# Kernel tuning notes

Measured on AMD Instinct MI355X. Metric: run time of the kernel, lower is better.

The kernel has to match this reference:

```python
import jax, jax.numpy as jnp
import numpy as np

N_SRC, N_TGT, E = 50000, 50000, 1600000
SRC_IN, TGT_IN, H, L = 64, 64, 128, 3
N = N_SRC + N_TGT


def setup_inputs() -> dict:
    key = jax.random.key(0)
    ks = jax.random.split(key, 12)
    s = 1.0 / np.sqrt(H)
    return {
        "src_x": jax.random.normal(ks[0], (N_SRC, SRC_IN), jnp.float32),
        "tgt_x": jax.random.normal(ks[1], (N_TGT, TGT_IN), jnp.float32),
        "edge_index": jax.random.randint(ks[2], (2, E), 0, N, jnp.int32),
        "Wsrc": jax.random.normal(ks[3], (H, SRC_IN), jnp.float32) / np.sqrt(SRC_IN),
        "bsrc": jnp.zeros((H,), jnp.float32),
        "Wtgt": jax.random.normal(ks[4], (H, TGT_IN), jnp.float32) / np.sqrt(TGT_IN),
        "btgt": jnp.zeros((H,), jnp.float32),
        "Wl": jax.random.normal(ks[5], (L, H, H), jnp.float32) * s,  # neighbor-aggregate weight
        "bl": jnp.zeros((L, H), jnp.float32),
        "Wr": jax.random.normal(ks[6], (L, H, H), jnp.float32) * s,  # root (self) weight, no bias
    }


def reference(src_x, tgt_x, edge_index, Wsrc, bsrc, Wtgt, btgt, Wl, bl, Wr):
    src_idx, dst_idx = edge_index[0], edge_index[1]
    # input projections + concat over node dim
    x = jnp.concatenate([src_x @ Wsrc.T + bsrc, tgt_x @ Wtgt.T + btgt], axis=0)  # [N,H]
    # in-degree for mean aggregation (computed once; edge structure is fixed)
    deg = jax.ops.segment_sum(jnp.ones((E,), x.dtype), dst_idx, num_segments=N)
    inv_deg = (1.0 / jnp.maximum(deg, 1.0))[:, None]  # [N,1]
    h = x
    for i in range(L):
        msg = h[src_idx]  # gather: [E,H]
        agg = jax.ops.segment_sum(msg, dst_idx, num_segments=N) * inv_deg  # mean aggr
        # PyG SAGEConv: lin_l(mean_neighbors) + lin_r(self); lin_l has bias
        h = agg @ Wl[i].T + bl[i] + h @ Wr[i].T
        if i + 1 < L:
            h = jax.nn.relu(h)  # dropout p=0.0 (eval) -> identity
    return h
```

## Files before the change

kernel.cpp:

```cpp
#include <hip/hip_runtime.h>
#include <hip/hip_fp8.h>

#define NSRC 50000
#define NTGT 50000
#define NTOT 100000
#define NE   1600000
#define IND  64
#define HD   128
#define CAP  64
#define CHUNK2 2048
#define NCH2 784
#define SBIN 128
#define NBIN 782
#define NBINP 784
#define PROJB 391
#define PACKB 48

typedef short s16x8 __attribute__((ext_vector_type(8)));
typedef float f32x4 __attribute__((ext_vector_type(4)));

__device__ __forceinline__ ushort f2bf(float f) {
  union { float f; uint u; } v; v.f = f;
  const uint r = v.u + 0x7fffu + ((v.u >> 16) & 1u);
  return (ushort)(r >> 16);
}
__device__ __forceinline__ float bfl(uint v) {
  union { uint u; float f; } c; c.u = v << 16; return c.f;
}
__device__ __forceinline__ float bfh(uint v) {
  union { uint u; float f; } c; c.u = v & 0xffff0000u; return c.f;
}
__device__ __forceinline__ int permj(int j) { return (j % 98) * 8 + j / 98; }

__device__ void pack_dev(const float* __restrict__ Wl, const float* __restrict__ Wr,
                         ushort* __restrict__ wpk, const int bid) {
  const int idx = bid * 256 + threadIdx.x;
  const int layer = idx >> 12;
  const int r = idx & 4095;
  const int which = r >> 11;
  const int g = r & 2047;
  const int cf = g >> 8;
  const int t = (g >> 6) & 3;
  const int lane = g & 63;
  const int lr = lane & 15;
  const int kc = (lane >> 4) * 8;
  const float* W = (which ? Wr : Wl) + (size_t)layer * HD * HD;
  const float* src = W + (size_t)(cf * 16 + lr) * HD + t * 32 + kc;
  const float4 a = *(const float4*)(src);
  const float4 b = *(const float4*)(src + 4);
  s16x8 o;
  o[0] = (short)f2bf(a.x); o[1] = (short)f2bf(a.y);
  o[2] = (short)f2bf(a.z); o[3] = (short)f2bf(a.w);
  o[4] = (short)f2bf(b.x); o[5] = (short)f2bf(b.y);
  o[6] = (short)f2bf(b.z); o[7] = (short)f2bf(b.w);
  *(s16x8*)(wpk + (size_t)idx * 8) = o;
}

__device__ void proj_dev(const float* __restrict__ x, const float* __restrict__ W,
                         const float* __restrict__ b, ushort* __restrict__ out,
                         const int count, const int out_base, const int bid) {
  const int lane = threadIdx.x & 63;
  const int wave = threadIdx.x >> 6;
  const int n0 = bid * 128 + wave * 32;
  const int lr = lane & 15;
  const int kc = (lane >> 4) * 8;
  const int rowq = (lane >> 4) * 4;

  s16x8 af[2][2];
#pragma unroll
  for (int r = 0; r < 2; ++r) {
    int ar = n0 + 16 * r + lr;
    if (ar >= count) ar = count - 1;
#pragma unroll
    for (int t = 0; t < 2; ++t) {
      const float* xp = x + (size_t)ar * IND + t * 32 + kc;
      const float4 xa = *(const float4*)(xp);
      const float4 xb = *(const float4*)(xp + 4);
      s16x8 a;
      a[0] = (short)f2bf(xa.x); a[1] = (short)f2bf(xa.y);
      a[2] = (short)f2bf(xa.z); a[3] = (short)f2bf(xa.w);
      a[4] = (short)f2bf(xb.x); a[5] = (short)f2bf(xb.y);
      a[6] = (short)f2bf(xb.z); a[7] = (short)f2bf(xb.w);
      af[r][t] = a;
    }
  }
#pragma unroll
  for (int cf = 0; cf < 8; ++cf) {
    const float* wp = W + (size_t)(cf * 16 + lr) * IND + kc;
    s16x8 w0, w1;
    {
      const float4 wa = *(const float4*)(wp);
      const float4 wb = *(const float4*)(wp + 4);
      const float4 wc = *(const float4*)(wp + 32);
      const float4 wd = *(const float4*)(wp + 36);
      w0[0] = (short)f2bf(wa.x); w0[1] = (short)f2bf(wa.y);
      w0[2] = (short)f2bf(wa.z); w0[3] = (short)f2bf(wa.w);
      w0[4] = (short)f2bf(wb.x); w0[5] = (short)f2bf(wb.y);
      w0[6] = (short)f2bf(wb.z); w0[7] = (short)f2bf(wb.w);
      w1[0] = (short)f2bf(wc.x); w1[1] = (short)f2bf(wc.y);
      w1[2] = (short)f2bf(wc.z); w1[3] = (short)f2bf(wc.w);
      w1[4] = (short)f2bf(wd.x); w1[5] = (short)f2bf(wd.y);
      w1[6] = (short)f2bf(wd.z); w1[7] = (short)f2bf(wd.w);
    }
    f32x4 acc0 = {0.f, 0.f, 0.f, 0.f};
    f32x4 acc1 = {0.f, 0.f, 0.f, 0.f};
    acc0 = __builtin_amdgcn_mfma_f32_16x16x32_bf16(af[0][0], w0, acc0, 0, 0, 0);
    acc1 = __builtin_amdgcn_mfma_f32_16x16x32_bf16(af[1][0], w0, acc1, 0, 0, 0);
    acc0 = __builtin_amdgcn_mfma_f32_16x16x32_bf16(af[0][1], w1, acc0, 0, 0, 0);
    acc1 = __builtin_amdgcn_mfma_f32_16x16x32_bf16(af[1][1], w1, acc1, 0, 0, 0);
    const int col = cf * 16 + lr;
    const float bv = b[col];
#pragma unroll
    for (int r = 0; r < 2; ++r) {
      const f32x4 acc = r ? acc1 : acc0;
#pragma unroll
      for (int q = 0; q < 4; ++q) {
        const int row = n0 + 16 * r + rowq + q;
        if (row < count) out[(size_t)(out_base + row) * HD + col] = f2bf(acc[q] + bv);
      }
    }
  }
}

__device__ void part2a_dev(const int* __restrict__ dst, uint* __restrict__ bincnt,
                           uint* __restrict__ histmat, const int bid) {
  __shared__ uint hist[NBIN];
  const int tid = threadIdx.x;
  const int i0 = bid * CHUNK2;
  const int i1 = (i0 + CHUNK2 < NE) ? i0 + CHUNK2 : NE;
  for (int j = tid; j < NBIN; j += 256) hist[j] = 0;
  __syncthreads();
  for (int i = i0 + tid; i < i1; i += 256)
    atomicAdd(&hist[((uint)dst[i]) >> 7], 1u);
  __syncthreads();
  for (int j = tid; j < NBIN; j += 256) {
    histmat[(size_t)bid * NBIN + j] = hist[j];
    if (hist[j]) atomicAdd(&bincnt[j], hist[j]);
  }
}

__global__ __launch_bounds__(256) void prep_kernel(
    const float* __restrict__ src_x, const float* __restrict__ tgt_x,
    const float* __restrict__ Wsrc, const float* __restrict__ bsrc,
    const float* __restrict__ Wtgt, const float* __restrict__ btgt,
    ushort* __restrict__ hbuf,
    const int* __restrict__ dst, uint* __restrict__ bincnt, uint* __restrict__ histmat,
    const float* __restrict__ Wl, const float* __restrict__ Wr,
    ushort* __restrict__ wpk) {
  const int b = blockIdx.x;
  if (b < PROJB) {
    proj_dev(src_x, Wsrc, bsrc, hbuf, NSRC, 0, b);
  } else if (b < 2 * PROJB) {
    proj_dev(tgt_x, Wtgt, btgt, hbuf, NTGT, NSRC, b - PROJB);
  } else if (b < 2 * PROJB + NCH2) {
    part2a_dev(dst, bincnt, histmat, b - 2 * PROJB);
  } else {
    pack_dev(Wl, Wr, wpk, b - 2 * PROJB - NCH2);
  }
}

__global__ __launch_bounds__(256) void scan_kernel(const uint* __restrict__ bincnt,
                                                   uint* __restrict__ binoff) {
  __shared__ uint lds[256];
  const int tid = threadIdx.x;
  uint v[4]; uint s = 0;
#pragma unroll
  for (int j = 0; j < 4; ++j) {
    const int idx = tid * 4 + j;
    v[j] = (idx < NBIN) ? bincnt[idx] : 0;
    s += v[j];
  }
  lds[tid] = s;
  __syncthreads();
  for (int off = 1; off < 256; off <<= 1) {
    const uint t = (tid >= off) ? lds[tid - off] : 0;
    __syncthreads();
    lds[tid] += t;
    __syncthreads();
  }
  uint run = lds[tid] - s;
#pragma unroll
  for (int j = 0; j < 4; ++j) {
    const int idx = tid * 4 + j;
    if (idx < NBIN) binoff[idx] = run;
    else if (idx == NBIN) binoff[idx] = run;
    run += v[j];
  }
}

__global__ __launch_bounds__(256) void colscan_kernel(const uint* __restrict__ histmat,
                                                      const uint* __restrict__ binoff,
                                                      uint* __restrict__ offmat) {
  const int bin = (blockIdx.x % 8) * 98 + blockIdx.x / 8;
  if (bin >= NBIN) return;
  __shared__ uint h[NCH2];
  __shared__ uint ps[256];
  const int tid = threadIdx.x;
  for (int j = tid; j < NCH2; j += 256)
    h[j] = histmat[(size_t)permj(j) * NBIN + bin];
  __syncthreads();
  uint s = 0;
  if (tid < 196) {
#pragma unroll
    for (int u = 0; u < 4; ++u) s += h[tid * 4 + u];
  }
  ps[tid] = s;
  __syncthreads();
  for (int off = 1; off < 256; off <<= 1) {
    const uint t = (tid >= off) ? ps[tid - off] : 0;
    __syncthreads();
    ps[tid] += t;
    __syncthreads();
  }
  if (tid < 196) {
    uint run = binoff[bin] + ps[tid] - s;
#pragma unroll
    for (int u = 0; u < 4; ++u) {
      const int j = tid * 4 + u;
      offmat[(size_t)permj(j) * NBIN + bin] = run;
      run += h[j];
    }
  }
}

__global__ __launch_bounds__(256) void part2b_kernel(const int* __restrict__ src, const int* __restrict__ dst,
                                                     const uint* __restrict__ offmat, uint* __restrict__ ebuf2) {
  __shared__ uint base[NBIN];
  __shared__ uint cur[NBIN];
  const int tid = threadIdx.x;
  const int bid = blockIdx.x;
  for (int j = tid; j < NBIN; j += 256) {
    base[j] = offmat[(size_t)bid * NBIN + j];
    cur[j] = 0;
  }
  __syncthreads();
  const int i0 = bid * CHUNK2;
  const int i1 = (i0 + CHUNK2 < NE) ? i0 + CHUNK2 : NE;
  for (int i = i0 + tid; i < i1; i += 256) {
    const uint d = (uint)dst[i];
    const uint bin = d >> 7;
    const uint pos = base[bin] + atomicAdd(&cur[bin], 1u);
    ebuf2[pos] = (uint)src[i] | ((d & 127u) << 17);
  }
}

__global__ __launch_bounds__(256) void part3_kernel(const uint* __restrict__ binoff, const uint* __restrict__ ebuf2,
                                                    uint* __restrict__ csr, int* __restrict__ rowstart) {
  __shared__ uint slotL[SBIN][CAP];
  __shared__ uint cntL[SBIN];
  __shared__ uint scanL[SBIN];
  const int tid = threadIdx.x;
  const int b = blockIdx.x;
  const int e0 = (int)binoff[b];
  const int e1 = (int)binoff[b + 1];
  for (int j = tid; j < SBIN; j += 256) cntL[j] = 0;
  __syncthreads();
  for (int i = e0 + tid; i < e1; i += 256) {
    const uint rec = ebuf2[i];
    const uint dl = rec >> 17;
    const uint pos = atomicAdd(&cntL[dl], 1u);
    if (pos < CAP) slotL[dl][pos] = rec & 0x1FFFFu;
  }
  __syncthreads();
  if (tid < SBIN) {
    uint cv = cntL[tid];
    scanL[tid] = cv < CAP ? cv : CAP;
  }
  __syncthreads();
  for (int off = 1; off < SBIN; off <<= 1) {
    uint t = 0;
    if (tid < SBIN && tid >= off) t = scanL[tid - off];
    __syncthreads();
    if (tid < SBIN) scanL[tid] += t;
    __syncthreads();
  }
  if (tid < SBIN) {
    const int node = b * SBIN + tid;
    const uint m = (cntL[tid] < CAP) ? cntL[tid] : CAP;
    const uint myoff = (uint)e0 + scanL[tid] - m;
    if (node < NTOT) {
      rowstart[node] = (int)myoff;
      for (uint j = 0; j < m; ++j) csr[myoff + j] = slotL[tid][j];
    }
  }
  if (b == NBIN - 1 && tid == 0) rowstart[NTOT] = e0 + (int)scanL[SBIN - 1];
}

__global__ __launch_bounds__(256) void cvt8_kernel(const ushort* __restrict__ h, uchar* __restrict__ h8) {
  const size_t idx = (size_t)blockIdx.x * 256 + threadIdx.x;
  const uint4 v = ((const uint4*)h)[idx];
  __hip_fp8x2_e4m3 q0(make_float2(bfl(v.x), bfh(v.x)));
  __hip_fp8x2_e4m3 q1(make_float2(bfl(v.y), bfh(v.y)));
  __hip_fp8x2_e4m3 q2(make_float2(bfl(v.z), bfh(v.z)));
  __hip_fp8x2_e4m3 q3(make_float2(bfl(v.w), bfh(v.w)));
  uint2 o;
  o.x = (uint)q0.__x | ((uint)q1.__x << 16);
  o.y = (uint)q2.__x | ((uint)q3.__x << 16);
  ((uint2*)h8)[idx] = o;
}

__global__ __launch_bounds__(256) void agg4_kernel(const uchar* __restrict__ h8, ushort* __restrict__ agg,
                                                   const int* __restrict__ rowstart, const uint* __restrict__ csr) {
  const int g = threadIdx.x >> 4;
  const int l16 = threadIdx.x & 15;
  const int n = blockIdx.x * 16 + g;
  const int r0 = rowstart[n];
  const int r1 = rowstart[n + 1];
  const uint2* hp = (const uint2*)h8;
  float a0 = 0.f, a1 = 0.f, a2 = 0.f, a3 = 0.f, a4 = 0.f, a5 = 0.f, a6 = 0.f, a7 = 0.f;
  __hip_fp8x2_e4m3 p;
#define ACC8(w) { \
    p.__x = (__hip_fp8x2_storage_t)((w).x & 0xFFFFu); { float2 f = (float2)p; a0 += f.x; a1 += f.y; } \
    p.__x = (__hip_fp8x2_storage_t)((w).x >> 16);     { float2 f = (float2)p; a2 += f.x; a3 += f.y; } \
    p.__x = (__hip_fp8x2_storage_t)((w).y & 0xFFFFu); { float2 f = (float2)p; a4 += f.x; a5 += f.y; } \
    p.__x = (__hip_fp8x2_storage_t)((w).y >> 16);     { float2 f = (float2)p; a6 += f.x; a7 += f.y; } }
  int i = r0;
  for (; i + 8 <= r1; i += 8) {
    uint s[8];
    uint2 v[8];
#pragma unroll
    for (int u = 0; u < 8; ++u) s[u] = csr[i + u];
#pragma unroll
    for (int u = 0; u < 8; ++u) v[u] = hp[(size_t)s[u] * 16 + l16];
#pragma unroll
    for (int u = 0; u < 8; ++u) ACC8(v[u]);
  }
  for (; i + 4 <= r1; i += 4) {
    uint s[4];
    uint2 v[4];
#pragma unroll
    for (int u = 0; u < 4; ++u) s[u] = csr[i + u];
#pragma unroll
    for (int u = 0; u < 4; ++u) v[u] = hp[(size_t)s[u] * 16 + l16];
#pragma unroll
    for (int u = 0; u < 4; ++u) ACC8(v[u]);
  }
  for (; i < r1; ++i) {
    const uint2 v = hp[(size_t)csr[i] * 16 + l16];
    ACC8(v);
  }
#undef ACC8
  const int deg = r1 - r0;
  const float sc = 1.0f / (float)(deg > 1 ? deg : 1);
  uint4 o;
  o.x = (uint)f2bf(a0 * sc) | ((uint)f2bf(a1 * sc) << 16);
  o.y = (uint)f2bf(a2 * sc) | ((uint)f2bf(a3 * sc) << 16);
  o.z = (uint)f2bf(a4 * sc) | ((uint)f2bf(a5 * sc) << 16);
  o.w = (uint)f2bf(a6 * sc) | ((uint)f2bf(a7 * sc) << 16);
  ((uint4*)agg)[(size_t)n * 16 + l16] = o;
}

__global__ __launch_bounds__(256) void mfma_gemm_kernel(
    const ushort* A, const ushort* Hm,
    const ushort* __restrict__ Wlp, const float* __restrict__ bl,
    const ushort* __restrict__ Wrp, void* outv, uchar* __restrict__ h8out,
    const int relu, const int f32out) {
  __shared__ ushort res[128][136];
  const int lane = threadIdx.x & 63;
  const int wave = threadIdx.x >> 6;
  const int n0 = blockIdx.x * 128;
  const int wrow = wave * 32;
  const int lr = lane & 15;
  const int kc = (lane >> 4) * 8;
  const int rowq = (lane >> 4) * 4;

  s16x8 af[2][4], hf[2][4];
#pragma unroll
  for (int r = 0; r < 2; ++r) {
    int ar = n0 + wrow + 16 * r + lr;
    if (ar >= NTOT) ar = NTOT - 1;
    const ushort* ap = A + (size_t)ar * HD + kc;
    const ushort* hp = Hm + (size_t)ar * HD + kc;
#pragma unroll
    for (int t = 0; t < 4; ++t) {
      af[r][t] = *(const s16x8*)(ap + t * 32);
      hf[r][t] = *(const s16x8*)(hp + t * 32);
    }
  }

  s16x8 wl[4], wr[4], wln[4], wrn[4];
#pragma unroll
  for (int t = 0; t < 4; ++t) {
    wl[t] = *(const s16x8*)(Wlp + (size_t)(t * 64 + lane) * 8);
    wr[t] = *(const s16x8*)(Wrp + (size_t)(t * 64 + lane) * 8);
  }
#pragma unroll
  for (int cf = 0; cf < 8; ++cf) {
    if (cf < 7) {
#pragma unroll
      for (int t = 0; t < 4; ++t) {
        wln[t] = *(const s16x8*)(Wlp + (size_t)(((cf + 1) * 4 + t) * 64 + lane) * 8);
        wrn[t] = *(const s16x8*)(Wrp + (size_t)(((cf + 1) * 4 + t) * 64 + lane) * 8);
      }
    }
    f32x4 acc0 = {0.f, 0.f, 0.f, 0.f};
    f32x4 acc1 = {0.f, 0.f, 0.f, 0.f};
#pragma unroll
    for (int t = 0; t < 4; ++t) {
      acc0 = __builtin_amdgcn_mfma_f32_16x16x32_bf16(af[0][t], wl[t], acc0, 0, 0, 0);
      acc1 = __builtin_amdgcn_mfma_f32_16x16x32_bf16(af[1][t], wl[t], acc1, 0, 0, 0);
      acc0 = __builtin_amdgcn_mfma_f32_16x16x32_bf16(hf[0][t], wr[t], acc0, 0, 0, 0);
      acc1 = __builtin_amdgcn_mfma_f32_16x16x32_bf16(hf[1][t], wr[t], acc1, 0, 0, 0);
    }
    const float bv = bl[cf * 16 + lr];
    const int col = cf * 16 + lr;
#pragma unroll
    for (int r = 0; r < 2; ++r) {
      const f32x4 acc = r ? acc1 : acc0;
#pragma unroll
      for (int q = 0; q < 4; ++q) {
        float v = acc[q] + bv;
        if (relu && v < 0.f) v = 0.f;
        res[wrow + 16 * r + rowq + q][col] = f2bf(v);
      }
    }
#pragma unroll
    for (int t = 0; t < 4; ++t) { wl[t] = wln[t]; wr[t] = wrn[t]; }
  }
  __syncthreads();
  const int tid = threadIdx.x;
#pragma unroll
  for (int k = 0; k < 8; ++k) {
    const int idx = k * 256 + tid;
    const int r = idx >> 4;
    const int c = idx & 15;
    const int grow = n0 + r;
    if (grow < NTOT) {
      const uint4 v = *(const uint4*)&res[r][c * 8];
      if (f32out) {
        float4 f0 = make_float4(bfl(v.x), bfh(v.x), bfl(v.y), bfh(v.y));
        float4 f1 = make_float4(bfl(v.z), bfh(v.z), bfl(v.w), bfh(v.w));
        ((float4*)outv)[(size_t)grow * 32 + c * 2] = f0;
        ((float4*)outv)[(size_t)grow * 32 + c * 2 + 1] = f1;
      } else {
        ((uint4*)outv)[(size_t)grow * 16 + c] = v;
        __hip_fp8x2_e4m3 q0(make_float2(bfl(v.x), bfh(v.x)));
        __hip_fp8x2_e4m3 q1(make_float2(bfl(v.y), bfh(v.y)));
        __hip_fp8x2_e4m3 q2(make_float2(bfl(v.z), bfh(v.z)));
        __hip_fp8x2_e4m3 q3(make_float2(bfl(v.w), bfh(v.w)));
        uint2 o;
        o.x = (uint)q0.__x | ((uint)q1.__x << 16);
        o.y = (uint)q2.__x | ((uint)q3.__x << 16);
        ((uint2*)h8out)[(size_t)grow * 16 + c] = o;
      }
    }
  }
}

extern "C" void kernel_launch(void* const* d_in, const int* in_sizes, int n_in,
                              void* d_out, int out_size, void* d_ws, size_t ws_size,
                              hipStream_t stream) {
  const float* src_x = (const float*)d_in[0];
  const float* tgt_x = (const float*)d_in[1];
  const int*   eidx  = (const int*)d_in[2];
  const float* Wsrc  = (const float*)d_in[3];
  const float* bsrc  = (const float*)d_in[4];
  const float* Wtgt  = (const float*)d_in[5];
  const float* btgt  = (const float*)d_in[6];
  const float* Wl    = (const float*)d_in[7];
  const float* bl    = (const float*)d_in[8];
  const float* Wr    = (const float*)d_in[9];
  float* out = (float*)d_out;
  (void)in_sizes; (void)n_in; (void)out_size; (void)ws_size;

  char* ws = (char*)d_ws;
  size_t off = 0;
  auto alloc = [&](size_t bytes) -> void* {
    void* p = (void*)(ws + off);
    off = (off + bytes + 511) & ~(size_t)511;
    return p;
  };
  ushort* hbuf   = (ushort*)alloc((size_t)NTOT * HD * sizeof(ushort));
  ushort* abuf   = (ushort*)alloc((size_t)NTOT * HD * sizeof(ushort));
  ushort* wpk    = (ushort*)alloc((size_t)3 * 2 * 2048 * 8 * sizeof(ushort));
  uint*   bincnt = (uint*)alloc(NBIN * sizeof(uint));
  uint*   binoff = (uint*)alloc((NBIN + 1) * sizeof(uint));

  uint*  dout_u   = (uint*)d_out;
  uint*  ebuf2    = dout_u;
  uint*  csr      = dout_u + 1700000;
  int*   rowstart = (int*)(dout_u + 3400000);
  uchar* h8buf    = (uchar*)(dout_u + 3600000);
  uint*  histmat  = dout_u + 6900000;
  uint*  offmat   = dout_u + 7600000;

  const int* src_idx = eidx;
  const int* dst_idx = eidx + NE;

  hipMemsetAsync(bincnt, 0, NBIN * sizeof(uint), stream);

  prep_kernel<<<2 * PROJB + NCH2 + PACKB, 256, 0, stream>>>(
      src_x, tgt_x, Wsrc, bsrc, Wtgt, btgt, hbuf, dst_idx, bincnt, histmat, Wl, Wr, wpk);

  scan_kernel<<<1, 256, 0, stream>>>(bincnt, binoff);
  colscan_kernel<<<NBINP, 256, 0, stream>>>(histmat, binoff, offmat);
  part2b_kernel<<<NCH2, 256, 0, stream>>>(src_idx, dst_idx, offmat, ebuf2);
  part3_kernel<<<NBIN, 256, 0, stream>>>(binoff, ebuf2, csr, rowstart);

  const int cgrid = NTOT * HD / 8 / 256;
  const int agrid = NTOT / 16;
  const int ggrid = (NTOT + 127) / 128;
  const size_t WPL = 2048 * 8;
  cvt8_kernel<<<cgrid, 256, 0, stream>>>(hbuf, h8buf);
  agg4_kernel<<<agrid, 256, 0, stream>>>(h8buf, abuf, rowstart, csr);
  mfma_gemm_kernel<<<ggrid, 256, 0, stream>>>(abuf, hbuf, wpk, bl, wpk + WPL, abuf, h8buf, 1, 0);
  agg4_kernel<<<agrid, 256, 0, stream>>>(h8buf, hbuf, rowstart, csr);
  mfma_gemm_kernel<<<ggrid, 256, 0, stream>>>(hbuf, abuf, wpk + 2 * WPL, bl + HD, wpk + 3 * WPL, hbuf, h8buf, 1, 0);
  agg4_kernel<<<agrid, 256, 0, stream>>>(h8buf, abuf, rowstart, csr);
  mfma_gemm_kernel<<<ggrid, 256, 0, stream>>>(abuf, hbuf, wpk + 4 * WPL, bl + 2 * HD, wpk + 5 * WPL, out, h8buf, 0, 1);
}
```

Baseline: 262.3 us.

## Fuse fp8 conversion into projection epilogue and drop global bin-count atomics

The input projection now stages its inputs and outputs through shared memory, so loads and stores are coalesced, and it writes the fp8 copy of h directly. This removes the separate cvt8 kernel launch and its extra read of hbuf. Per-bin totals now come out of the column scan instead of global atomics, which removes the memset. Bin offsets are added inside part2b rather than in colscan. The cost is a large shared-memory allocation in prep_kernel that every block reserves, including the histogram and pack blocks, which may reduce occupancy.

```diff
diff --git a/kernel.cpp b/kernel.cpp
--- a/kernel.cpp
+++ b/kernel.cpp
@@ -58,32 +58,34 @@
 
 __device__ void proj_dev(const float* __restrict__ x, const float* __restrict__ W,
                          const float* __restrict__ b, ushort* __restrict__ out,
-                         const int count, const int out_base, const int bid) {
-  const int lane = threadIdx.x & 63;
-  const int wave = threadIdx.x >> 6;
-  const int n0 = bid * 128 + wave * 32;
+                         uchar* __restrict__ h8, const int count, const int out_base,
+                         const int bid, ushort* smem) {
+  ushort (*xt)[72] = (ushort(*)[72])smem;
+  ushort (*res)[136] = (ushort(*)[136])smem;
+  const int tid = threadIdx.x;
+  const int n0 = bid * 128;
+#pragma unroll
+  for (int k = 0; k < 32; ++k) {
+    const int idx = k * 256 + tid;
+    const int row = idx >> 6;
+    const int col = idx & 63;
+    int gr = n0 + row; if (gr >= count) gr = count - 1;
+    xt[row][col] = f2bf(x[(size_t)gr * IND + col]);
+  }
+  __syncthreads();
+  const int lane = tid & 63;
+  const int wave = tid >> 6;
+  const int wrow = wave * 32;
   const int lr = lane & 15;
   const int kc = (lane >> 4) * 8;
   const int rowq = (lane >> 4) * 4;
-
   s16x8 af[2][2];
 #pragma unroll
-  for (int r = 0; r < 2; ++r) {
-    int ar = n0 + 16 * r + lr;
-    if (ar >= count) ar = count - 1;
-#pragma unroll
-    for (int t = 0; t < 2; ++t) {
-      const float* xp = x + (size_t)ar * IND + t * 32 + kc;
-      const float4 xa = *(const float4*)(xp);
-      const float4 xb = *(const float4*)(xp + 4);
-      s16x8 a;
-      a[0] = (short)f2bf(xa.x); a[1] = (short)f2bf(xa.y);
-      a[2] = (short)f2bf(xa.z); a[3] = (short)f2bf(xa.w);
-      a[4] = (short)f2bf(xb.x); a[5] = (short)f2bf(xb.y);
-      a[6] = (short)f2bf(xb.z); a[7] = (short)f2bf(xb.w);
-      af[r][t] = a;
-    }
-  }
+  for (int r = 0; r < 2; ++r)
+#pragma unroll
+    for (int t = 0; t < 2; ++t)
+      af[r][t] = *(const s16x8*)&xt[wrow + 16 * r + lr][t * 32 + kc];
+  __syncthreads();
 #pragma unroll
   for (int cf = 0; cf < 8; ++cf) {
     const float* wp = W + (size_t)(cf * 16 + lr) * IND + kc;
@@ -114,16 +116,33 @@
     for (int r = 0; r < 2; ++r) {
       const f32x4 acc = r ? acc1 : acc0;
 #pragma unroll
-      for (int q = 0; q < 4; ++q) {
-        const int row = n0 + 16 * r + rowq + q;
-        if (row < count) out[(size_t)(out_base + row) * HD + col] = f2bf(acc[q] + bv);
-      }
-    }
-  }
-}
-
-__device__ void part2a_dev(const int* __restrict__ dst, uint* __restrict__ bincnt,
-                           uint* __restrict__ histmat, const int bid) {
+      for (int q = 0; q < 4; ++q)
+        res[wrow + 16 * r + rowq + q][col] = f2bf(acc[q] + bv);
+    }
+  }
+  __syncthreads();
+#pragma unroll
+  for (int k = 0; k < 8; ++k) {
+    const int idx = k * 256 + tid;
+    const int r = idx >> 4;
+    const int c = idx & 15;
+    const int grow = n0 + r;
+    if (grow < count) {
+      const uint4 v = *(const uint4*)&res[r][c * 8];
+      ((uint4*)out)[(size_t)(out_base + grow) * 16 + c] = v;
+      __hip_fp8x2_e4m3 q0(make_float2(bfl(v.x), bfh(v.x)));
+      __hip_fp8x2_e4m3 q1(make_float2(bfl(v.y), bfh(v.y)));
+      __hip_fp8x2_e4m3 q2(make_float2(bfl(v.z), bfh(v.z)));
+      __hip_fp8x2_e4m3 q3(make_float2(bfl(v.w), bfh(v.w)));
+      uint2 o;
+      o.x = (uint)q0.__x | ((uint)q1.__x << 16);
+      o.y = (uint)q2.__x | ((uint)q3.__x << 16);
+      ((uint2*)h8)[(size_t)(out_base + grow) * 16 + c] = o;
+    }
+  }
+}
+
+__device__ void part2a_dev(const int* __restrict__ dst, uint* __restrict__ histmat, const int bid) {
   __shared__ uint hist[NBIN];
   const int tid = threadIdx.x;
   const int i0 = bid * CHUNK2;
@@ -133,33 +152,68 @@
   for (int i = i0 + tid; i < i1; i += 256)
     atomicAdd(&hist[((uint)dst[i]) >> 7], 1u);
   __syncthreads();
-  for (int j = tid; j < NBIN; j += 256) {
+  for (int j = tid; j < NBIN; j += 256)
     histmat[(size_t)bid * NBIN + j] = hist[j];
-    if (hist[j]) atomicAdd(&bincnt[j], hist[j]);
-  }
 }
 
 __global__ __launch_bounds__(256) void prep_kernel(
     const float* __restrict__ src_x, const float* __restrict__ tgt_x,
     const float* __restrict__ Wsrc, const float* __restrict__ bsrc,
     const float* __restrict__ Wtgt, const float* __restrict__ btgt,
-    ushort* __restrict__ hbuf,
-    const int* __restrict__ dst, uint* __restrict__ bincnt, uint* __restrict__ histmat,
+    ushort* __restrict__ hbuf, uchar* __restrict__ h8buf,
+    const int* __restrict__ dst, uint* __restrict__ histmat,
     const float* __restrict__ Wl, const float* __restrict__ Wr,
     ushort* __restrict__ wpk) {
+  __shared__ ushort smem[128 * 136];
   const int b = blockIdx.x;
   if (b < PROJB) {
-    proj_dev(src_x, Wsrc, bsrc, hbuf, NSRC, 0, b);
+    proj_dev(src_x, Wsrc, bsrc, hbuf, h8buf, NSRC, 0, b, smem);
   } else if (b < 2 * PROJB) {
-    proj_dev(tgt_x, Wtgt, btgt, hbuf, NTGT, NSRC, b - PROJB);
+    proj_dev(tgt_x, Wtgt, btgt, hbuf, h8buf, NTGT, NSRC, b - PROJB, smem);
   } else if (b < 2 * PROJB + NCH2) {
-    part2a_dev(dst, bincnt, histmat, b - 2 * PROJB);
+    part2a_dev(dst, histmat, b - 2 * PROJB);
   } else {
     pack_dev(Wl, Wr, wpk, b - 2 * PROJB - NCH2);
   }
 }
 
-__global__ __launch_bounds__(256) void scan_kernel(const uint* __restrict__ bincnt,
+__global__ __launch_bounds__(256) void colscan_kernel(const uint* __restrict__ histmat,
+                                                      uint* __restrict__ offmat,
+                                                      uint* __restrict__ bintot) {
+  const int bin = (blockIdx.x % 8) * 98 + blockIdx.x / 8;
+  if (bin >= NBIN) return;
+  __shared__ uint h[NCH2];
+  __shared__ uint ps[256];
+  const int tid = threadIdx.x;
+  for (int j = tid; j < NCH2; j += 256)
+    h[j] = histmat[(size_t)permj(j) * NBIN + bin];
+  __syncthreads();
+  uint s = 0;
+  if (tid < 196) {
+#pragma unroll
+    for (int u = 0; u < 4; ++u) s += h[tid * 4 + u];
+  }
+  ps[tid] = s;
+  __syncthreads();
+  for (int off = 1; off < 256; off <<= 1) {
+    const uint t = (tid >= off) ? ps[tid - off] : 0;
+    __syncthreads();
+    ps[tid] += t;
+    __syncthreads();
+  }
+  if (tid < 196) {
+    uint run = ps[tid] - s;
+#pragma unroll
+    for (int u = 0; u < 4; ++u) {
+      const int j = tid * 4 + u;
+      offmat[(size_t)permj(j) * NBIN + bin] = run;
+      run += h[j];
+    }
+  }
+  if (tid == 255) bintot[bin] = ps[255];
+}
+
+__global__ __launch_bounds__(256) void scan_kernel(const uint* __restrict__ bintot,
                                                    uint* __restrict__ binoff) {
   __shared__ uint lds[256];
   const int tid = threadIdx.x;
@@ -167,7 +221,7 @@
 #pragma unroll
   for (int j = 0; j < 4; ++j) {
     const int idx = tid * 4 + j;
-    v[j] = (idx < NBIN) ? bincnt[idx] : 0;
+    v[j] = (idx < NBIN) ? bintot[idx] : 0;
     s += v[j];
   }
   lds[tid] = s;
@@ -188,49 +242,16 @@
   }
 }
 
-__global__ __launch_bounds__(256) void colscan_kernel(const uint* __restrict__ histmat,
-                                                      const uint* __restrict__ binoff,
-                                                      uint* __restrict__ offmat) {
-  const int bin = (blockIdx.x % 8) * 98 + blockIdx.x / 8;
-  if (bin >= NBIN) return;
-  __shared__ uint h[NCH2];
-  __shared__ uint ps[256];
-  const int tid = threadIdx.x;
-  for (int j = tid; j < NCH2; j += 256)
-    h[j] = histmat[(size_t)permj(j) * NBIN + bin];
-  __syncthreads();
-  uint s = 0;
-  if (tid < 196) {
-#pragma unroll
-    for (int u = 0; u < 4; ++u) s += h[tid * 4 + u];
-  }
-  ps[tid] = s;
-  __syncthreads();
-  for (int off = 1; off < 256; off <<= 1) {
-    const uint t = (tid >= off) ? ps[tid - off] : 0;
-    __syncthreads();
-    ps[tid] += t;
-    __syncthreads();
-  }
-  if (tid < 196) {
-    uint run = binoff[bin] + ps[tid] - s;
-#pragma unroll
-    for (int u = 0; u < 4; ++u) {
-      const int j = tid * 4 + u;
-      offmat[(size_t)permj(j) * NBIN + bin] = run;
-      run += h[j];
-    }
-  }
-}
-
 __global__ __launch_bounds__(256) void part2b_kernel(const int* __restrict__ src, const int* __restrict__ dst,
-                                                     const uint* __restrict__ offmat, uint* __restrict__ ebuf2) {
+                                                     const uint* __restrict__ offmat,
+                                                     const uint* __restrict__ binoff,
+                                                     uint* __restrict__ ebuf2) {
   __shared__ uint base[NBIN];
   __shared__ uint cur[NBIN];
   const int tid = threadIdx.x;
   const int bid = blockIdx.x;
   for (int j = tid; j < NBIN; j += 256) {
-    base[j] = offmat[(size_t)bid * NBIN + j];
+    base[j] = offmat[(size_t)bid * NBIN + j] + binoff[j];
     cur[j] = 0;
   }
   __syncthreads();
@@ -284,19 +305,6 @@
     }
   }
   if (b == NBIN - 1 && tid == 0) rowstart[NTOT] = e0 + (int)scanL[SBIN - 1];
-}
-
-__global__ __launch_bounds__(256) void cvt8_kernel(const ushort* __restrict__ h, uchar* __restrict__ h8) {
-  const size_t idx = (size_t)blockIdx.x * 256 + threadIdx.x;
-  const uint4 v = ((const uint4*)h)[idx];
-  __hip_fp8x2_e4m3 q0(make_float2(bfl(v.x), bfh(v.x)));
-  __hip_fp8x2_e4m3 q1(make_float2(bfl(v.y), bfh(v.y)));
-  __hip_fp8x2_e4m3 q2(make_float2(bfl(v.z), bfh(v.z)));
-  __hip_fp8x2_e4m3 q3(make_float2(bfl(v.w), bfh(v.w)));
-  uint2 o;
-  o.x = (uint)q0.__x | ((uint)q1.__x << 16);
-  o.y = (uint)q2.__x | ((uint)q3.__x << 16);
-  ((uint2*)h8)[idx] = o;
 }
 
 __global__ __launch_bounds__(256) void agg4_kernel(const uchar* __restrict__ h8, ushort* __restrict__ agg,
@@ -473,7 +481,7 @@
   ushort* hbuf   = (ushort*)alloc((size_t)NTOT * HD * sizeof(ushort));
   ushort* abuf   = (ushort*)alloc((size_t)NTOT * HD * sizeof(ushort));
   ushort* wpk    = (ushort*)alloc((size_t)3 * 2 * 2048 * 8 * sizeof(ushort));
-  uint*   bincnt = (uint*)alloc(NBIN * sizeof(uint));
+  uint*   bintot = (uint*)alloc(NBIN * sizeof(uint));
   uint*   binoff = (uint*)alloc((NBIN + 1) * sizeof(uint));
 
   uint*  dout_u   = (uint*)d_out;
@@ -487,21 +495,17 @@
   const int* src_idx = eidx;
   const int* dst_idx = eidx + NE;
 
-  hipMemsetAsync(bincnt, 0, NBIN * sizeof(uint), stream);
-
   prep_kernel<<<2 * PROJB + NCH2 + PACKB, 256, 0, stream>>>(
-      src_x, tgt_x, Wsrc, bsrc, Wtgt, btgt, hbuf, dst_idx, bincnt, histmat, Wl, Wr, wpk);
-
-  scan_kernel<<<1, 256, 0, stream>>>(bincnt, binoff);
-  colscan_kernel<<<NBINP, 256, 0, stream>>>(histmat, binoff, offmat);
-  part2b_kernel<<<NCH2, 256, 0, stream>>>(src_idx, dst_idx, offmat, ebuf2);
+      src_x, tgt_x, Wsrc, bsrc, Wtgt, btgt, hbuf, h8buf, dst_idx, histmat, Wl, Wr, wpk);
+
+  colscan_kernel<<<NBINP, 256, 0, stream>>>(histmat, offmat, bintot);
+  scan_kernel<<<1, 256, 0, stream>>>(bintot, binoff);
+  part2b_kernel<<<NCH2, 256, 0, stream>>>(src_idx, dst_idx, offmat, binoff, ebuf2);
   part3_kernel<<<NBIN, 256, 0, stream>>>(binoff, ebuf2, csr, rowstart);
 
-  const int cgrid = NTOT * HD / 8 / 256;
   const int agrid = NTOT / 16;
   const int ggrid = (NTOT + 127) / 128;
   const size_t WPL = 2048 * 8;
-  cvt8_kernel<<<cgrid, 256, 0, stream>>>(hbuf, h8buf);
   agg4_kernel<<<agrid, 256, 0, stream>>>(h8buf, abuf, rowstart, csr);
   mfma_gemm_kernel<<<ggrid, 256, 0, stream>>>(abuf, hbuf, wpk, bl, wpk + WPL, abuf, h8buf, 1, 0);
   agg4_kernel<<<agrid, 256, 0, stream>>>(h8buf, hbuf, rowstart, csr);
```

Measured after the change: 246.4 us. 6.1% less time.
